# Performance work log

Hardware: AMD Instinct MI355X
Metric: run time of the kernel (lower is better)

The kernel has to match this reference:

```python
import jax, jax.numpy as jnp
import numpy as np

B, R, NT = 1, 384, 4        # batch, num_res, num_templates
C_IN = 128                   # rep_2d num_c (pair channels)
C_KV = 64                    # template pair channels
H, C = 4, 64                 # num_heads, attention_num_c


def setup_inputs() -> dict:
    key = jax.random.key(0)
    ks = jax.random.split(key, 7)
    s = lambda fan_in: 1.0 / np.sqrt(fan_in)
    return {
        "z2d": jax.random.normal(ks[0], (B, R, R, C_IN), jnp.float32),
        "t2d": jax.random.normal(ks[1], (B, NT, R, R, C_KV), jnp.float32),
        # weights stored [in, out] (torch nn.Linear applies x @ W.T)
        "Wq": jax.random.normal(ks[2], (C_IN, H * C), jnp.float32) * s(C_IN),
        "Wk": jax.random.normal(ks[3], (C_KV, H * C), jnp.float32) * s(C_KV),
        "Wv": jax.random.normal(ks[4], (C_KV, H * C), jnp.float32) * s(C_KV),
        "Wo": jax.random.normal(ks[5], (H * C, C_IN), jnp.float32) * s(H * C),
        "bo": jax.random.normal(ks[6], (C_IN,), jnp.float32) * s(H * C),
    }


def reference(z2d, t2d, Wq, Wk, Wv, Wo, bo):
    b, r, _, c_in = z2d.shape
    nt = t2d.shape[1]
    P = r * r  # flattened residue-pair axis

    z = z2d.reshape(b, P, 1, c_in)                             # [b, P, 1, c_in]
    t = jnp.transpose(t2d, (0, 2, 3, 1, 4)).reshape(b, P, nt, -1)  # [b, P, K, c_kv]

    q = (z @ Wq).reshape(b, P, 1, H, C) * C ** (-0.5)          # [b, P, 1, h, c]
    k = (t @ Wk).reshape(b, P, nt, H, C)                       # [b, P, k, h, c]
    v = (t @ Wv).reshape(b, P, nt, H, C)

    logits = jnp.einsum('bpqhc,bpkhc->bphqk', q, k)            # softmax over k templates
    weights = jax.nn.softmax(logits, axis=-1)
    weighted_avg = jnp.einsum('bphqk,bpkhc->bpqhc', weights, v)  # [b, P, 1, h, c]

    out = weighted_avg.reshape(b, P, 1, H * C) @ Wo + bo
    return out.reshape(b, r, r, c_in)
```

## Files before the change

### kernel.cpp

```cpp
#include <hip/hip_runtime.h>

#define R_   384
#define P_   (R_ * R_)
#define NT_  4
#define CIN  128
#define CKV  64
#define NH   4
#define HC   256

#define TP   64
#define LDZ  136
#define LDT  264

typedef __attribute__((ext_vector_type(8))) short bf16x8;
typedef __attribute__((ext_vector_type(4))) float f32x4;
typedef __attribute__((ext_vector_type(4))) uint  u32x4;

__device__ __forceinline__ ushort f2bf_s(float f) {
    uint32_t u = __float_as_uint(f);
    u += 0x7FFFu + ((u >> 16) & 1u);
    return (ushort)(u >> 16);
}
__device__ __forceinline__ uint packbf2(float lo, float hi) {
    return (uint)f2bf_s(lo) | ((uint)f2bf_s(hi) << 16);
}
__device__ __forceinline__ uint2 pack4(const float4 v) {
    uint2 r; r.x = packbf2(v.x, v.y); r.y = packbf2(v.z, v.w); return r;
}
__device__ __forceinline__ float bflo(uint t) { return __uint_as_float(t << 16); }
__device__ __forceinline__ float bfhi(uint t) { return __uint_as_float(t & 0xffff0000u); }

__global__ __launch_bounds__(256) void precompute_mg(
        const float* __restrict__ Wq, const float* __restrict__ Wk,
        const float* __restrict__ Wv, const float* __restrict__ Wo,
        ushort* __restrict__ Mt, ushort* __restrict__ Gt) {
    int tid = blockIdx.x * blockDim.x + threadIdx.x;
    if (tid < HC * CIN) {
        int n = tid >> 7, ci = tid & 127;
        int h = n >> 6, j = n & 63;
        float acc = 0.f;
        for (int c = 0; c < 64; ++c)
            acc += Wq[ci * HC + h * 64 + c] * Wk[j * HC + h * 64 + c];
        int jp = ((j >> 2) & 3) * 16 + (j >> 4) * 4 + (j & 3);
        Mt[(h * 64 + jp) * CIN + ci] = f2bf_s(acc * 0.125f);
    } else {
        int t = tid - HC * CIN;
        int co = t >> 8, n = t & 255;
        int h = n >> 6, j = n & 63;
        float acc = 0.f;
        for (int c = 0; c < 64; ++c)
            acc += Wv[j * HC + h * 64 + c] * Wo[(h * 64 + c) * CIN + co];
        Gt[co * HC + n] = f2bf_s(acc);
    }
}

__global__ __launch_bounds__(256, 3) void tpa_fused(
        const float* __restrict__ z2d, const float* __restrict__ t2d,
        const ushort* __restrict__ Mt, const ushort* __restrict__ Gt,
        const float* __restrict__ bo, float* __restrict__ out) {

    __shared__ ushort s0[TP * LDZ];
    __shared__ ushort sT[TP * LDT];

    const int tid  = threadIdx.x;
    const int lane = tid & 63;
    const int wv   = tid >> 6;
    const int lr   = lane & 15;
    const int g    = lane >> 4;
    const int g8   = g << 3;
    const int pg0  = blockIdx.x * TP;

    bf16x8 B1[4][4];
    #pragma unroll
    for (int kt = 0; kt < 4; ++kt)
        #pragma unroll
        for (int nt = 0; nt < 4; ++nt)
            B1[kt][nt] = *(const bf16x8*)(Mt + (wv * 64 + nt * 16 + lr) * CIN + kt * 32 + g8);

    #pragma unroll
    for (int i = 0; i < 8; ++i) {
        int idx = (i * 256 + tid) * 4, p = idx >> 7, c = idx & 127;
        float4 v = *(const float4*)(z2d + (size_t)(pg0 + p) * CIN + c);
        *(uint2*)&s0[p * LDZ + c] = pack4(v);
    }
    #pragma unroll
    for (int k = 0; k < NT_; ++k) {
        const float* src = t2d + ((size_t)k * P_ + pg0) * CKV;
        #pragma unroll
        for (int i = 0; i < 4; ++i) {
            int idx = (i * 256 + tid) * 4, p = idx >> 6, c = idx & 63;
            float4 v = *(const float4*)(src + p * 64 + c);
            *(uint2*)&sT[p * LDT + k * 64 + c] = pack4(v);
        }
    }
    __syncthreads();

    f32x4 acc1[4][4];
    #pragma unroll
    for (int nt = 0; nt < 4; ++nt)
        #pragma unroll
        for (int mt = 0; mt < 4; ++mt)
            acc1[nt][mt] = (f32x4){0.f, 0.f, 0.f, 0.f};
    #pragma unroll
    for (int kt = 0; kt < 4; ++kt) {
        bf16x8 zf[4];
        #pragma unroll
        for (int mt = 0; mt < 4; ++mt)
            zf[mt] = *(const bf16x8*)&s0[(mt * 16 + lr) * LDZ + kt * 32 + g8];
        #pragma unroll
        for (int nt = 0; nt < 4; ++nt)
            #pragma unroll
            for (int mt = 0; mt < 4; ++mt)
                acc1[nt][mt] = __builtin_amdgcn_mfma_f32_16x16x32_bf16(
                    B1[kt][nt], zf[mt], acc1[nt][mt], 0, 0, 0);
    }

    bf16x8 B2[8][2];
    #pragma unroll
    for (int kt = 0; kt < 8; ++kt)
        #pragma unroll
        for (int nt = 0; nt < 2; ++nt)
            B2[kt][nt] = *(const bf16x8*)(Gt + (wv * 32 + nt * 16 + lr) * HC + kt * 32 + g8);
    const float bias0 = bo[wv * 32 + lr];
    const float bias1 = bo[wv * 32 + 16 + lr];

    u32x4 ureg[4][2];
    #pragma unroll
    for (int mt = 0; mt < 4; ++mt) {
        const int p = mt * 16 + lr;
        u32x4 tq[NT_][2];
        #pragma unroll
        for (int k = 0; k < NT_; ++k) {
            tq[k][0] = *(const u32x4*)&sT[p * LDT + k * 64 + g * 16];
            tq[k][1] = *(const u32x4*)&sT[p * LDT + k * 64 + g * 16 + 8];
        }
        float lg[4];
        #pragma unroll
        for (int k = 0; k < NT_; ++k) {
            float s = 0.f;
            #pragma unroll
            for (int nt = 0; nt < 4; ++nt)
                #pragma unroll
                for (int r = 0; r < 4; ++r) {
                    int cc = nt * 4 + r;
                    uint tw = tq[k][cc >> 3][(cc >> 1) & 3];
                    float tv = (cc & 1) ? bfhi(tw) : bflo(tw);
                    s = fmaf(acc1[nt][mt][r], tv, s);
                }
            s += __shfl_xor(s, 16);
            s += __shfl_xor(s, 32);
            lg[k] = s;
        }
        float mx = fmaxf(fmaxf(lg[0], lg[1]), fmaxf(lg[2], lg[3]));
        float w0 = __expf(lg[0] - mx), w1 = __expf(lg[1] - mx);
        float w2 = __expf(lg[2] - mx), w3 = __expf(lg[3] - mx);
        float inv = 1.f / (w0 + w1 + w2 + w3);
        w0 *= inv; w1 *= inv; w2 *= inv; w3 *= inv;

        #pragma unroll
        for (int j = 0; j < 2; ++j) {
            u32x4 o;
            #pragma unroll
            for (int e = 0; e < 4; ++e) {
                uint t0 = tq[0][j][e], t1 = tq[1][j][e];
                uint t2 = tq[2][j][e], t3 = tq[3][j][e];
                float lo = w0 * bflo(t0) + w1 * bflo(t1) + w2 * bflo(t2) + w3 * bflo(t3);
                float hi = w0 * bfhi(t0) + w1 * bfhi(t1) + w2 * bfhi(t2) + w3 * bfhi(t3);
                o[e] = packbf2(lo, hi);
            }
            ureg[mt][j] = o;
        }
    }
    __syncthreads();

    #pragma unroll
    for (int mt = 0; mt < 4; ++mt) {
        const int p = mt * 16 + lr;
        *(u32x4*)&sT[p * LDT + wv * 64 + g * 16]     = ureg[mt][0];
        *(u32x4*)&sT[p * LDT + wv * 64 + g * 16 + 8] = ureg[mt][1];
    }
    __syncthreads();

    f32x4 acc2[4][2];
    #pragma unroll
    for (int mt = 0; mt < 4; ++mt)
        #pragma unroll
        for (int nt = 0; nt < 2; ++nt)
            acc2[mt][nt] = (f32x4){0.f, 0.f, 0.f, 0.f};
    #pragma unroll
    for (int kt = 0; kt < 8; ++kt) {
        bf16x8 af[4];
        #pragma unroll
        for (int mt = 0; mt < 4; ++mt)
            af[mt] = *(const bf16x8*)&sT[(mt * 16 + lr) * LDT + kt * 32 + g8];
        #pragma unroll
        for (int mt = 0; mt < 4; ++mt)
            #pragma unroll
            for (int nt = 0; nt < 2; ++nt)
                acc2[mt][nt] = __builtin_amdgcn_mfma_f32_16x16x32_bf16(
                    af[mt], B2[kt][nt], acc2[mt][nt], 0, 0, 0);
    }

    #pragma unroll
    for (int nt = 0; nt < 2; ++nt) {
        int co = wv * 32 + nt * 16 + lr;
        float bias = nt ? bias1 : bias0;
        #pragma unroll
        for (int mt = 0; mt < 4; ++mt) {
            int row = mt * 16 + g * 4;
            #pragma unroll
            for (int r = 0; r < 4; ++r)
                out[(size_t)(pg0 + row + r) * CIN + co] = acc2[mt][nt][r] + bias;
        }
    }
}

extern "C" void kernel_launch(void* const* d_in, const int* in_sizes, int n_in,
                              void* d_out, int out_size, void* d_ws, size_t ws_size,
                              hipStream_t stream) {
    const float* z2d = (const float*)d_in[0];
    const float* t2d = (const float*)d_in[1];
    const float* Wq  = (const float*)d_in[2];
    const float* Wk  = (const float*)d_in[3];
    const float* Wv  = (const float*)d_in[4];
    const float* Wo  = (const float*)d_in[5];
    const float* bo  = (const float*)d_in[6];

    ushort* Mt = (ushort*)d_ws;
    ushort* Gt = Mt + HC * CIN;

    precompute_mg<<<(2 * HC * CIN) / 256, 256, 0, stream>>>(Wq, Wk, Wv, Wo, Mt, Gt);
    tpa_fused<<<P_ / TP, 256, 0, stream>>>(z2d, t2d, Mt, Gt, bo, (float*)d_out);
}
```

Measured before the change: 78.57 us.

## Load z directly into MFMA fragments, drop z LDS tile, vectorize output stores

Removes the shared-memory staging buffer for the z tile. Each lane now reads its MFMA operand straight from global memory and converts it to bf16 in registers, which lowers LDS usage enough to raise the occupancy hint from 3 to 4 blocks. The second GEMM swaps its operand order so each lane holds 4 consecutive output channels, which allows float4 output stores and float4 bias loads instead of scalar strided stores. The costs are uncoalesced 32-byte global reads for z, the pipeline barrier moving after the first GEMM, and tighter register pressure at the higher occupancy.

```diff
diff --git a/kernel.cpp b/kernel.cpp
--- a/kernel.cpp
+++ b/kernel.cpp
@@ -9,7 +9,6 @@
 #define HC   256
 
 #define TP   64
-#define LDZ  136
 #define LDT  264
 
 typedef __attribute__((ext_vector_type(8))) short bf16x8;
@@ -29,6 +28,8 @@
 }
 __device__ __forceinline__ float bflo(uint t) { return __uint_as_float(t << 16); }
 __device__ __forceinline__ float bfhi(uint t) { return __uint_as_float(t & 0xffff0000u); }
+
+union BF8 { bf16x8 v; uint u[4]; };
 
 __global__ __launch_bounds__(256) void precompute_mg(
         const float* __restrict__ Wq, const float* __restrict__ Wk,
@@ -54,12 +55,11 @@
     }
 }
 
-__global__ __launch_bounds__(256, 3) void tpa_fused(
+__global__ __launch_bounds__(256, 4) void tpa_fused(
         const float* __restrict__ z2d, const float* __restrict__ t2d,
         const ushort* __restrict__ Mt, const ushort* __restrict__ Gt,
         const float* __restrict__ bo, float* __restrict__ out) {
 
-    __shared__ ushort s0[TP * LDZ];
     __shared__ ushort sT[TP * LDT];
 
     const int tid  = threadIdx.x;
@@ -78,12 +78,6 @@
             B1[kt][nt] = *(const bf16x8*)(Mt + (wv * 64 + nt * 16 + lr) * CIN + kt * 32 + g8);
 
     #pragma unroll
-    for (int i = 0; i < 8; ++i) {
-        int idx = (i * 256 + tid) * 4, p = idx >> 7, c = idx & 127;
-        float4 v = *(const float4*)(z2d + (size_t)(pg0 + p) * CIN + c);
-        *(uint2*)&s0[p * LDZ + c] = pack4(v);
-    }
-    #pragma unroll
     for (int k = 0; k < NT_; ++k) {
         const float* src = t2d + ((size_t)k * P_ + pg0) * CKV;
         #pragma unroll
@@ -93,7 +87,6 @@
             *(uint2*)&sT[p * LDT + k * 64 + c] = pack4(v);
         }
     }
-    __syncthreads();
 
     f32x4 acc1[4][4];
     #pragma unroll
@@ -105,8 +98,15 @@
     for (int kt = 0; kt < 4; ++kt) {
         bf16x8 zf[4];
         #pragma unroll
-        for (int mt = 0; mt < 4; ++mt)
-            zf[mt] = *(const bf16x8*)&s0[(mt * 16 + lr) * LDZ + kt * 32 + g8];
+        for (int mt = 0; mt < 4; ++mt) {
+            const float* zp = z2d + (size_t)(pg0 + mt * 16 + lr) * CIN + kt * 32 + g8;
+            float4 z0 = *(const float4*)zp;
+            float4 z1 = *(const float4*)(zp + 4);
+            BF8 zb;
+            zb.u[0] = packbf2(z0.x, z0.y); zb.u[1] = packbf2(z0.z, z0.w);
+            zb.u[2] = packbf2(z1.x, z1.y); zb.u[3] = packbf2(z1.z, z1.w);
+            zf[mt] = zb.v;
+        }
         #pragma unroll
         for (int nt = 0; nt < 4; ++nt)
             #pragma unroll
@@ -114,6 +114,7 @@
                 acc1[nt][mt] = __builtin_amdgcn_mfma_f32_16x16x32_bf16(
                     B1[kt][nt], zf[mt], acc1[nt][mt], 0, 0, 0);
     }
+    __syncthreads();
 
     bf16x8 B2[8][2];
     #pragma unroll
@@ -121,8 +122,10 @@
         #pragma unroll
         for (int nt = 0; nt < 2; ++nt)
             B2[kt][nt] = *(const bf16x8*)(Gt + (wv * 32 + nt * 16 + lr) * HC + kt * 32 + g8);
-    const float bias0 = bo[wv * 32 + lr];
-    const float bias1 = bo[wv * 32 + 16 + lr];
+    float4 b4[2];
+    #pragma unroll
+    for (int nt = 0; nt < 2; ++nt)
+        b4[nt] = *(const float4*)(bo + wv * 32 + nt * 16 + g * 4);
 
     u32x4 ureg[4][2];
     #pragma unroll
@@ -181,36 +184,38 @@
     }
     __syncthreads();
 
-    f32x4 acc2[4][2];
-    #pragma unroll
-    for (int mt = 0; mt < 4; ++mt)
+    f32x4 acc2[2][4];
+    #pragma unroll
+    for (int nt = 0; nt < 2; ++nt)
+        #pragma unroll
+        for (int mt = 0; mt < 4; ++mt)
+            acc2[nt][mt] = (f32x4){0.f, 0.f, 0.f, 0.f};
+    #pragma unroll
+    for (int kt = 0; kt < 8; ++kt) {
+        bf16x8 uf[4];
+        #pragma unroll
+        for (int mt = 0; mt < 4; ++mt)
+            uf[mt] = *(const bf16x8*)&sT[(mt * 16 + lr) * LDT + kt * 32 + g8];
         #pragma unroll
         for (int nt = 0; nt < 2; ++nt)
-            acc2[mt][nt] = (f32x4){0.f, 0.f, 0.f, 0.f};
-    #pragma unroll
-    for (int kt = 0; kt < 8; ++kt) {
-        bf16x8 af[4];
-        #pragma unroll
-        for (int mt = 0; mt < 4; ++mt)
-            af[mt] = *(const bf16x8*)&sT[(mt * 16 + lr) * LDT + kt * 32 + g8];
-        #pragma unroll
-        for (int mt = 0; mt < 4; ++mt)
-            #pragma unroll
-            for (int nt = 0; nt < 2; ++nt)
-                acc2[mt][nt] = __builtin_amdgcn_mfma_f32_16x16x32_bf16(
-                    af[mt], B2[kt][nt], acc2[mt][nt], 0, 0, 0);
+            #pragma unroll
+            for (int mt = 0; mt < 4; ++mt)
+                acc2[nt][mt] = __builtin_amdgcn_mfma_f32_16x16x32_bf16(
+                    B2[kt][nt], uf[mt], acc2[nt][mt], 0, 0, 0);
     }
 
     #pragma unroll
     for (int nt = 0; nt < 2; ++nt) {
-        int co = wv * 32 + nt * 16 + lr;
-        float bias = nt ? bias1 : bias0;
+        int co0 = wv * 32 + nt * 16 + g * 4;
         #pragma unroll
         for (int mt = 0; mt < 4; ++mt) {
-            int row = mt * 16 + g * 4;
-            #pragma unroll
-            for (int r = 0; r < 4; ++r)
-                out[(size_t)(pg0 + row + r) * CIN + co] = acc2[mt][nt][r] + bias;
+            int p = mt * 16 + lr;
+            float4 o;
+            o.x = acc2[nt][mt][0] + b4[nt].x;
+            o.y = acc2[nt][mt][1] + b4[nt].y;
+            o.z = acc2[nt][mt][2] + b4[nt].z;
+            o.w = acc2[nt][mt][3] + b4[nt].w;
+            *(float4*)(out + (size_t)(pg0 + p) * CIN + co0) = o;
         }
     }
 }
```

New measurement: 191.7 us. +143.9%, slower.
